# Kernel tuning notes

Hardware: AMD Instinct MI355X
Metric: run time of the kernel (lower is better)

Reference implementation:

```python
import jax, jax.numpy as jnp
import numpy as np

B, LC, LQ, D = 64, 1024, 128, 128
NEG_BIG = 1.0e12


def _len_mask(seq_len, T):
    # seq_len: (B,1) int. Equivalent to 1 - cumsum(one_hot(L, T)): 1 for pos < L.
    pos = jnp.arange(T)  # (T,)
    return (pos[None, :] < seq_len).astype(jnp.float32)  # (B,T)


def setup_inputs() -> dict:
    key = jax.random.key(0)
    ks = jax.random.split(key, 7)
    return {
        "x_cont": jax.random.normal(ks[0], (B, LC, D), dtype=jnp.float32),
        "x_ques": jax.random.normal(ks[1], (B, LQ, D), dtype=jnp.float32),
        "W0": jax.random.normal(ks[2], (D, 1), dtype=jnp.float32) / np.sqrt(D),
        "W1": jax.random.normal(ks[3], (D, 1), dtype=jnp.float32) / np.sqrt(D),
        "W2": jax.random.normal(ks[4], (1, 1, D), dtype=jnp.float32) / np.sqrt(D),
        "cont_len": jax.random.randint(ks[5], (B, 1), 1, LC, dtype=jnp.int32),
        "ques_len": jax.random.randint(ks[6], (B, 1), 1, LQ, dtype=jnp.int32),
    }


def reference(x_cont, x_ques, W0, W1, W2, cont_len, ques_len):
    # Trilinear similarity: S[b,c,q] = x_cont@W0 + x_ques@W1 + (x_cont*W2) . x_ques
    s_cont = jnp.einsum('bcd,do->bco', x_cont, W0)            # (B,LC,1)
    s_ques = jnp.einsum('bqd,do->boq', x_ques, W1)            # (B,1,LQ)
    s_fuse = jnp.einsum('bcd,bqd->bcq', x_cont * W2, x_ques)  # (B,LC,LQ)
    S = s_cont + s_ques + s_fuse                               # (B,LC,LQ)

    mask_q = _len_mask(ques_len, LQ)  # (B,LQ)
    mask_c = _len_mask(cont_len, LC)  # (B,LC)

    # Softmax over query axis, masking invalid query positions (axis=-1)
    S_bar = jax.nn.softmax(S - (1.0 - mask_q)[:, None, :] * NEG_BIG, axis=-1)
    # Softmax over context axis, masking invalid context positions, then transpose
    S_T = jnp.swapaxes(
        jax.nn.softmax(S - (1.0 - mask_c)[:, :, None] * NEG_BIG, axis=1), 1, 2
    )  # (B,LQ,LC)

    c2q = jnp.einsum('bcq,bqd->bcd', S_bar, x_ques)             # (B,LC,D)
    q2c = jnp.einsum('bcq,bqk,bkd->bcd', S_bar, S_T, x_cont)    # (B,LC,D)

    result = jnp.concatenate(
        [x_cont, c2q, x_cont * c2q, x_cont * q2c], axis=-1
    )  # (B,LC,4D)
    return result, S_bar, S_T
```

## Files before the change

kernel.cpp:

```cpp
#include <hip/hip_runtime.h>

#define NB 64
#define LC 1024
#define LQ 128
#define DD 128
#define NEG_BIG 1.0e12f

typedef __attribute__((ext_vector_type(8))) short short8;
typedef __attribute__((ext_vector_type(4))) unsigned short ushort4v;
typedef __attribute__((ext_vector_type(4))) float floatx4;

__device__ __forceinline__ unsigned short f2bf(float f) {
  union { float f; unsigned int u; } v;
  v.f = f;
  const unsigned int r = v.u + 0x7FFFu + ((v.u >> 16) & 1u);
  return (unsigned short)(r >> 16);
}
__device__ __forceinline__ float bf2f(unsigned int u) {
  union { unsigned int u; float f; } v;
  v.u = u << 16;
  return v.f;
}

#define PADW 136

__global__ __launch_bounds__(512) void k_score(
    const float* __restrict__ xc, const float* __restrict__ xq,
    const float* __restrict__ w2, const float* __restrict__ W0,
    const float* __restrict__ W1, const int* __restrict__ qlen_p,
    const int* __restrict__ clen_p, float* __restrict__ out_sbar,
    unsigned short* __restrict__ Pb, float* __restrict__ colsum_part,
    unsigned short* __restrict__ xcT, unsigned short* __restrict__ xqT,
    unsigned short* __restrict__ sbarb) {
  __shared__ __align__(16) unsigned short smem[2 * 128 * PADW];
  __shared__ float a_cont_s[128];
  __shared__ float a_ques_s[128];
  unsigned short* xcs = smem;
  unsigned short* xqs = smem + 128 * PADW;
  unsigned short* ptile = smem + 128 * PADW;

  const int b = blockIdx.x >> 3;
  const int ct = blockIdx.x & 7;
  const int c0 = ct << 7;
  const int t = threadIdx.x;
  const int w = t >> 6, lane = t & 63;
  const int frow = lane & 15;
  const int kb = lane >> 4;

  const float* xc_blk = xc + ((size_t)b * LC + c0) * DD;
  const float* xq_b = xq + (size_t)b * LQ * DD;

  const int u = t & 15;
  const float4 w0a = *(const float4*)(W0 + (u << 3));
  const float4 w0b = *(const float4*)(W0 + (u << 3) + 4);
  const float4 w1a = *(const float4*)(W1 + (u << 3));
  const float4 w1b = *(const float4*)(W1 + (u << 3) + 4);
  const float4 w2a = *(const float4*)(w2 + (u << 3));
  const float4 w2b = *(const float4*)(w2 + (u << 3) + 4);

#pragma unroll
  for (int i = 0; i < 4; ++i) {
    const int row = (t >> 4) + (i << 5);
    {
      const float4 v0 = *(const float4*)(xc_blk + (size_t)row * DD + (u << 3));
      const float4 v1 = *(const float4*)(xc_blk + (size_t)row * DD + (u << 3) + 4);
      short8 pk;
      pk[0] = (short)f2bf(v0.x); pk[1] = (short)f2bf(v0.y);
      pk[2] = (short)f2bf(v0.z); pk[3] = (short)f2bf(v0.w);
      pk[4] = (short)f2bf(v1.x); pk[5] = (short)f2bf(v1.y);
      pk[6] = (short)f2bf(v1.z); pk[7] = (short)f2bf(v1.w);
      *(short8*)(xcs + row * PADW + (u << 3)) = pk;
      float pd = v0.x * w0a.x + v0.y * w0a.y + v0.z * w0a.z + v0.w * w0a.w +
                 v1.x * w0b.x + v1.y * w0b.y + v1.z * w0b.z + v1.w * w0b.w;
#pragma unroll
      for (int msk = 8; msk >= 1; msk >>= 1) pd += __shfl_xor(pd, msk, 64);
      if ((lane & 15) == 0) a_cont_s[row] = pd;
    }
    {
      const float4 v0 = *(const float4*)(xq_b + (size_t)row * DD + (u << 3));
      const float4 v1 = *(const float4*)(xq_b + (size_t)row * DD + (u << 3) + 4);
      float pq = v0.x * w1a.x + v0.y * w1a.y + v0.z * w1a.z + v0.w * w1a.w +
                 v1.x * w1b.x + v1.y * w1b.y + v1.z * w1b.z + v1.w * w1b.w;
#pragma unroll
      for (int msk = 8; msk >= 1; msk >>= 1) pq += __shfl_xor(pq, msk, 64);
      if ((lane & 15) == 0) a_ques_s[row] = pq;
      short8 pk;
      pk[0] = (short)f2bf(v0.x * w2a.x); pk[1] = (short)f2bf(v0.y * w2a.y);
      pk[2] = (short)f2bf(v0.z * w2a.z); pk[3] = (short)f2bf(v0.w * w2a.w);
      pk[4] = (short)f2bf(v1.x * w2b.x); pk[5] = (short)f2bf(v1.y * w2b.y);
      pk[6] = (short)f2bf(v1.z * w2b.z); pk[7] = (short)f2bf(v1.w * w2b.w);
      *(short8*)(xqs + row * PADW + (u << 3)) = pk;
    }
  }

  const int qlen = qlen_p[b];
  const int clen = clen_p[b];

  __syncthreads();

  float ac[4], aq[8];
#pragma unroll
  for (int reg = 0; reg < 4; ++reg)
    ac[reg] = a_cont_s[w * 16 + kb * 4 + reg];
#pragma unroll
  for (int n = 0; n < 8; ++n) aq[n] = a_ques_s[n * 16 + frow];

  floatx4 acc[8];
#pragma unroll
  for (int n = 0; n < 8; ++n) acc[n] = (floatx4){0.f, 0.f, 0.f, 0.f};
  const unsigned short* arow = xcs + (w * 16 + frow) * PADW + kb * 8;
  const unsigned short* brow = xqs + frow * PADW + kb * 8;
#pragma unroll
  for (int ks = 0; ks < 4; ++ks) {
    const short8 af = *(const short8*)(arow + ks * 32);
#pragma unroll
    for (int n = 0; n < 8; ++n) {
      const short8 bf = *(const short8*)(brow + n * 16 * PADW + ks * 32);
      acc[n] = __builtin_amdgcn_mfma_f32_16x16x32_bf16(af, bf, acc[n], 0, 0, 0);
    }
  }

  {
    const int d = t & 127;
    const int half = t >> 7;
    __align__(16) unsigned short tmp[32];
#pragma unroll
    for (int j = 0; j < 32; ++j)
      tmp[j] = xcs[((half << 5) + j) * PADW + d];
    unsigned short* dp = xcT + ((size_t)b * DD + d) * LC + c0 + (half << 5);
#pragma unroll
    for (int j = 0; j < 4; ++j)
      *(short8*)(dp + (j << 3)) = *(const short8*)(tmp + (j << 3));
  }

  float raw[8][4];
#pragma unroll
  for (int n = 0; n < 8; ++n)
#pragma unroll
    for (int reg = 0; reg < 4; ++reg) raw[n][reg] = acc[n][reg] + ac[reg] + aq[n];

  float mreg[4], invreg[4];
  float* sbar_row0 =
      out_sbar + ((size_t)b * LC + c0 + w * 16 + kb * 4) * LQ + frow;
#pragma unroll
  for (int reg = 0; reg < 4; ++reg) {
    float x[8];
    float m = -3.4e38f;
#pragma unroll
    for (int n = 0; n < 8; ++n) {
      x[n] = raw[n][reg] - ((n * 16 + frow) < qlen ? 0.f : NEG_BIG);
      m = fmaxf(m, x[n]);
    }
#pragma unroll
    for (int msk = 8; msk >= 1; msk >>= 1) m = fmaxf(m, __shfl_xor(m, msk, 64));
    float s = 0.f;
#pragma unroll
    for (int n = 0; n < 8; ++n) {
      x[n] = __expf(x[n] - m);
      s += x[n];
    }
#pragma unroll
    for (int msk = 8; msk >= 1; msk >>= 1) s += __shfl_xor(s, msk, 64);
    const float inv = 1.0f / s;
    float* o = sbar_row0 + (size_t)reg * LQ;
#pragma unroll
    for (int n = 0; n < 8; ++n) o[n * 16] = x[n] * inv;
    mreg[reg] = m;
    invreg[reg] = inv;
  }

  unsigned short* sb_out = sbarb + ((size_t)b * LC + c0) * LQ;
#pragma unroll
  for (int p = 0; p < 4; ++p) {
    __syncthreads();
    if ((w >> 1) == p) {
      const int crow = ((w & 1) << 4) + (kb << 2);
#pragma unroll
      for (int reg = 0; reg < 4; ++reg) {
        const float m = mreg[reg], inv = invreg[reg];
#pragma unroll
        for (int n = 0; n < 8; ++n) {
          const float xv = raw[n][reg] - ((n * 16 + frow) < qlen ? 0.f : NEG_BIG);
          ptile[(crow + reg) * 136 + (n << 4) + frow] = f2bf(__expf(xv - m) * inv);
        }
      }
    }
    __syncthreads();
    const int row = t >> 4, ch = t & 15;
    *(short8*)(sb_out + (size_t)((p << 5) + row) * LQ + (ch << 3)) =
        *(const short8*)(ptile + row * 136 + (ch << 3));
  }

  const int cl0 = c0 + w * 16 + kb * 4;
#pragma unroll
  for (int reg = 0; reg < 4; ++reg) {
    const bool ok = (cl0 + reg) < clen;
#pragma unroll
    for (int n = 0; n < 8; ++n)
      raw[n][reg] = ok ? __expf(raw[n][reg]) : 0.f;
  }

  unsigned short* Pb_b = Pb + (size_t)b * LQ * LC;
  float* cs_blk = colsum_part + ((size_t)b * 8 + ct) * LQ;
#pragma unroll
  for (int p = 0; p < 4; ++p) {
    __syncthreads();
#pragma unroll
    for (int n2 = 0; n2 < 2; ++n2) {
#pragma unroll
      for (int reg = 0; reg < 4; ++reg)
        ptile[(n2 * 16 + frow) * 136 + (w * 16 + kb * 4 + reg)] =
            f2bf(raw[2 * p + n2][reg]);
    }
    __syncthreads();
    const int qrow = t >> 4;
    const int ch = t & 15;
    const short8 pv = *(const short8*)(ptile + qrow * 136 + (ch << 3));
    *(short8*)(Pb_b + (size_t)(p * 32 + qrow) * LC + c0 + (ch << 3)) = pv;
    float s = 0.f;
#pragma unroll
    for (int j = 0; j < 8; ++j) s += bf2f((unsigned short)pv[j]);
#pragma unroll
    for (int msk = 8; msk >= 1; msk >>= 1) s += __shfl_xor(s, msk, 64);
    if (ch == 0) cs_blk[p * 32 + qrow] = s;
  }

  if (ct == 0) {
    __syncthreads();
#pragma unroll
    for (int i = 0; i < 4; ++i) {
      const int id = t + (i << 9);
      const int row = id >> 4, uu = id & 15;
      const float4 v0 = *(const float4*)(xq_b + (size_t)row * DD + (uu << 3));
      const float4 v1 = *(const float4*)(xq_b + (size_t)row * DD + (uu << 3) + 4);
      short8 pk;
      pk[0] = (short)f2bf(v0.x); pk[1] = (short)f2bf(v0.y);
      pk[2] = (short)f2bf(v0.z); pk[3] = (short)f2bf(v0.w);
      pk[4] = (short)f2bf(v1.x); pk[5] = (short)f2bf(v1.y);
      pk[6] = (short)f2bf(v1.z); pk[7] = (short)f2bf(v1.w);
      *(short8*)(ptile + row * 136 + (uu << 3)) = pk;
    }
    __syncthreads();
    const int d = t >> 2, ch4 = t & 3;
    __align__(16) unsigned short tmp2[32];
#pragma unroll
    for (int j = 0; j < 32; ++j)
      tmp2[j] = ptile[(ch4 * 32 + j) * 136 + d];
    unsigned short* dp = xqT + ((size_t)b * DD + d) * LQ + ch4 * 32;
#pragma unroll
    for (int j = 0; j < 4; ++j)
      *(short8*)(dp + (j << 3)) = *(const short8*)(tmp2 + (j << 3));
  }
}

__global__ __launch_bounds__(256) void k_fuse(
    const unsigned short* __restrict__ Pb, const float* __restrict__ colsum_part,
    const unsigned short* __restrict__ xcT, float* __restrict__ st,
    unsigned short* __restrict__ AbT) {
  __shared__ __align__(16) unsigned short Ps[16 * 1032];
  __shared__ unsigned short abt[128 * 20];
  __shared__ float inv_s[16];

  const int b = blockIdx.x >> 3;
  const int q0 = (blockIdx.x & 7) << 4;
  const int t = threadIdx.x;
  const int w = t >> 6, lane = t & 63;
  const int frow = lane & 15, kb = lane >> 4;

  const unsigned short* Pb_blk = Pb + ((size_t)b * LQ + q0) * LC;
  {
    const int row = t >> 4;
#pragma unroll
    for (int j = 0; j < 8; ++j) {
      const int cs = ((t & 15) << 3) + (j << 7);
      *(short8*)(Ps + row * 1032 + cs) =
          *(const short8*)(Pb_blk + (size_t)row * LC + cs);
    }
  }
  if (t < 16) {
    float s = 0.f;
#pragma unroll
    for (int j = 0; j < 8; ++j)
      s += colsum_part[((size_t)b * 8 + j) * LQ + q0 + t];
    inv_s[t] = 1.0f / s;
  }
  __syncthreads();

  {
    const int row = t >> 4;
    const float inv = inv_s[row];
    float* dst = st + ((size_t)b * LQ + q0 + row) * LC;
#pragma unroll
    for (int j = 0; j < 8; ++j) {
      const int cs = ((t & 15) << 3) + (j << 7);
      const short8 pv = *(const short8*)(Ps + row * 1032 + cs);
      float4 o0, o1;
      o0.x = bf2f((unsigned short)pv[0]) * inv;
      o0.y = bf2f((unsigned short)pv[1]) * inv;
      o0.z = bf2f((unsigned short)pv[2]) * inv;
      o0.w = bf2f((unsigned short)pv[3]) * inv;
      o1.x = bf2f((unsigned short)pv[4]) * inv;
      o1.y = bf2f((unsigned short)pv[5]) * inv;
      o1.z = bf2f((unsigned short)pv[6]) * inv;
      o1.w = bf2f((unsigned short)pv[7]) * inv;
      *(float4*)(dst + cs) = o0;
      *(float4*)(dst + cs + 4) = o1;
    }
  }

  const unsigned short* xcT_b = xcT + (size_t)b * DD * LC;
  const unsigned short* b0p =
      xcT_b + (size_t)((w * 2 + 0) * 16 + frow) * LC + kb * 8;
  const unsigned short* b1p =
      xcT_b + (size_t)((w * 2 + 1) * 16 + frow) * LC + kb * 8;
  const unsigned short* ap = Ps + frow * 1032 + kb * 8;
  floatx4 acc0 = (floatx4){0.f, 0.f, 0.f, 0.f};
  floatx4 acc1 = (floatx4){0.f, 0.f, 0.f, 0.f};
#pragma unroll 8
  for (int kk = 0; kk < 32; ++kk) {
    const short8 af = *(const short8*)(ap + kk * 32);
    const short8 b0 = *(const short8*)(b0p + kk * 32);
    const short8 b1 = *(const short8*)(b1p + kk * 32);
    acc0 = __builtin_amdgcn_mfma_f32_16x16x32_bf16(af, b0, acc0, 0, 0, 0);
    acc1 = __builtin_amdgcn_mfma_f32_16x16x32_bf16(af, b1, acc1, 0, 0, 0);
  }

  __syncthreads();
  const float i0 = inv_s[kb * 4 + 0], i1 = inv_s[kb * 4 + 1];
  const float i2 = inv_s[kb * 4 + 2], i3 = inv_s[kb * 4 + 3];
  {
    const int d0 = (w * 2 + 0) * 16 + frow;
    abt[d0 * 20 + kb * 4 + 0] = f2bf(acc0[0] * i0);
    abt[d0 * 20 + kb * 4 + 1] = f2bf(acc0[1] * i1);
    abt[d0 * 20 + kb * 4 + 2] = f2bf(acc0[2] * i2);
    abt[d0 * 20 + kb * 4 + 3] = f2bf(acc0[3] * i3);
    const int d1 = (w * 2 + 1) * 16 + frow;
    abt[d1 * 20 + kb * 4 + 0] = f2bf(acc1[0] * i0);
    abt[d1 * 20 + kb * 4 + 1] = f2bf(acc1[1] * i1);
    abt[d1 * 20 + kb * 4 + 2] = f2bf(acc1[2] * i2);
    abt[d1 * 20 + kb * 4 + 3] = f2bf(acc1[3] * i3);
  }
  __syncthreads();
  const int d = t >> 1, h = t & 1;
  short8 ov;
#pragma unroll
  for (int j = 0; j < 8; ++j)
    ((unsigned short*)&ov)[j] = abt[d * 20 + h * 8 + j];
  *(short8*)(AbT + ((size_t)b * DD + d) * LQ + q0 + h * 8) = ov;
}

__global__ __launch_bounds__(256) void k_out(
    const float* __restrict__ xc, const unsigned short* __restrict__ sbarb,
    const unsigned short* __restrict__ xqT, const unsigned short* __restrict__ AbT,
    float* __restrict__ out) {
  __shared__ __align__(16) float stg[2 * 32 * 132];

  const int b = blockIdx.x >> 4;
  const int c0 = (blockIdx.x & 15) << 6;
  const int t = threadIdx.x;
  const int w = t >> 6, lane = t & 63;
  const int frow = lane & 15, kb = lane >> 4;

  const unsigned short* sb_blk = sbarb + ((size_t)b * LC + c0) * LQ;
  const unsigned short* xqT_b = xqT + (size_t)b * DD * LQ;
  const unsigned short* AbT_b = AbT + (size_t)b * DD * LQ;
  short8 bq[2][4], ba[2][4];
#pragma unroll
  for (int nt = 0; nt < 2; ++nt) {
    const int d = (w << 5) + (nt << 4) + frow;
#pragma unroll
    for (int ks = 0; ks < 4; ++ks) {
      bq[nt][ks] = *(const short8*)(xqT_b + (size_t)d * LQ + ks * 32 + kb * 8);
      ba[nt][ks] = *(const short8*)(AbT_b + (size_t)d * LQ + ks * 32 + kb * 8);
    }
  }

  floatx4 accq[4][2], acca[4][2];
#pragma unroll
  for (int mt = 0; mt < 4; ++mt)
#pragma unroll
    for (int nt = 0; nt < 2; ++nt) {
      accq[mt][nt] = (floatx4){0.f, 0.f, 0.f, 0.f};
      acca[mt][nt] = (floatx4){0.f, 0.f, 0.f, 0.f};
    }
#pragma unroll
  for (int mt = 0; mt < 4; ++mt) {
#pragma unroll
    for (int ks = 0; ks < 4; ++ks) {
      const short8 af = *(const short8*)(
          sb_blk + (size_t)((mt << 4) + frow) * LQ + ks * 32 + kb * 8);
#pragma unroll
      for (int nt = 0; nt < 2; ++nt) {
        accq[mt][nt] =
            __builtin_amdgcn_mfma_f32_16x16x32_bf16(af, bq[nt][ks], accq[mt][nt], 0, 0, 0);
        acca[mt][nt] =
            __builtin_amdgcn_mfma_f32_16x16x32_bf16(af, ba[nt][ks], acca[mt][nt], 0, 0, 0);
      }
    }
  }

  float* out_b = out + ((size_t)b * LC + c0) * (4 * DD);
  const float* xc_blk = xc + ((size_t)b * LC + c0) * DD;

#pragma unroll
  for (int p = 0; p < 2; ++p) {
    __syncthreads();
#pragma unroll
    for (int mh = 0; mh < 2; ++mh) {
      const int mt = 2 * p + mh;
#pragma unroll
      for (int nt = 0; nt < 2; ++nt) {
        const int d = (w << 5) + (nt << 4) + frow;
        const int cl = (mh << 4) + (kb << 2);
#pragma unroll
        for (int reg = 0; reg < 4; ++reg) {
          stg[(cl + reg) * 132 + d] = accq[mt][nt][reg];
          stg[32 * 132 + (cl + reg) * 132 + d] = acca[mt][nt][reg];
        }
      }
    }
    __syncthreads();
    const int g = lane >> 4;
    const int d0 = (lane & 15) << 3;
#pragma unroll
    for (int j = 0; j < 8; ++j) {
      const int rl = (w << 3) + j;
      const int c = (p << 5) + rl;
      const float4 xv0 = *(const float4*)(xc_blk + (size_t)c * DD + d0);
      const float4 xv1 = *(const float4*)(xc_blk + (size_t)c * DD + d0 + 4);
      const float4 cq0 = *(const float4*)(stg + rl * 132 + d0);
      const float4 cq1 = *(const float4*)(stg + rl * 132 + d0 + 4);
      const float4 qc0 = *(const float4*)(stg + 32 * 132 + rl * 132 + d0);
      const float4 qc1 = *(const float4*)(stg + 32 * 132 + rl * 132 + d0 + 4);
      float4 o0, o1;
      if (g == 0) { o0 = xv0; o1 = xv1; }
      else if (g == 1) { o0 = cq0; o1 = cq1; }
      else if (g == 2) {
        o0 = make_float4(xv0.x * cq0.x, xv0.y * cq0.y, xv0.z * cq0.z, xv0.w * cq0.w);
        o1 = make_float4(xv1.x * cq1.x, xv1.y * cq1.y, xv1.z * cq1.z, xv1.w * cq1.w);
      } else {
        o0 = make_float4(xv0.x * qc0.x, xv0.y * qc0.y, xv0.z * qc0.z, xv0.w * qc0.w);
        o1 = make_float4(xv1.x * qc1.x, xv1.y * qc1.y, xv1.z * qc1.z, xv1.w * qc1.w);
      }
      float* o = out_b + (size_t)c * (4 * DD) + (g << 7) + d0;
      *(float4*)(o) = o0;
      *(float4*)(o + 4) = o1;
    }
  }
}

extern "C" void kernel_launch(void* const* d_in, const int* in_sizes, int n_in,
                              void* d_out, int out_size, void* d_ws, size_t ws_size,
                              hipStream_t stream) {
  const float* xc = (const float*)d_in[0];
  const float* xq = (const float*)d_in[1];
  const float* W0 = (const float*)d_in[2];
  const float* W1 = (const float*)d_in[3];
  const float* W2 = (const float*)d_in[4];
  const int* clen = (const int*)d_in[5];
  const int* qlen = (const int*)d_in[6];

  float* out = (float*)d_out;
  float* out_sbar = out + (size_t)NB * LC * 4 * DD;
  float* out_st = out_sbar + (size_t)NB * LC * LQ;

  float* colsum_part = (float*)d_ws;
  unsigned short* xcT = (unsigned short*)(colsum_part + NB * 8 * LQ);
  unsigned short* xqT = xcT + (size_t)NB * LC * DD;
  unsigned short* AbT = xqT + (size_t)NB * LQ * DD;
  unsigned short* Pb = AbT + (size_t)NB * LQ * DD;
  unsigned short* sbarb = Pb + (size_t)NB * LQ * LC;

  k_score<<<NB * 8, 512, 0, stream>>>(xc, xq, W2, W0, W1, qlen, clen,
                                      out_sbar, Pb, colsum_part, xcT, xqT,
                                      sbarb);
  k_fuse<<<NB * 8, 256, 0, stream>>>(Pb, colsum_part, xcT, out_st, AbT);
  k_out<<<NB * 16, 256, 0, stream>>>(xc, sbarb, xqT, AbT, out);
}
```

Before: 114.6 us.

## Coalesce S_bar and P stores via single LDS tile, move xqT transpose to k_fuse

The S_bar softmax epilogue now stages the whole 128x128 bf16 tile in LDS once and writes both the bf16 copy and the fp32 output with row-contiguous vector stores. Previously the fp32 store was strided per lane and the bf16 store went through four staged passes. The P/column-sum writeback likewise uses one full-tile LDS transpose with fewer barriers. The x_ques transpose that only ct==0 blocks did is moved into k_fuse, split across all blocks, to remove the load imbalance in k_score. The fp32 S_bar output is now derived from bf16-rounded values, which loses precision.

Result: slower. 127.4 us (+11.2%).

```diff
diff --git a/kernel.cpp b/kernel.cpp
--- a/kernel.cpp
+++ b/kernel.cpp
@@ -30,8 +30,7 @@
     const float* __restrict__ W1, const int* __restrict__ qlen_p,
     const int* __restrict__ clen_p, float* __restrict__ out_sbar,
     unsigned short* __restrict__ Pb, float* __restrict__ colsum_part,
-    unsigned short* __restrict__ xcT, unsigned short* __restrict__ xqT,
-    unsigned short* __restrict__ sbarb) {
+    unsigned short* __restrict__ xcT, unsigned short* __restrict__ sbarb) {
   __shared__ __align__(16) unsigned short smem[2 * 128 * PADW];
   __shared__ float a_cont_s[128];
   __shared__ float a_ques_s[128];
@@ -140,8 +139,6 @@
     for (int reg = 0; reg < 4; ++reg) raw[n][reg] = acc[n][reg] + ac[reg] + aq[n];
 
   float mreg[4], invreg[4];
-  float* sbar_row0 =
-      out_sbar + ((size_t)b * LC + c0 + w * 16 + kb * 4) * LQ + frow;
 #pragma unroll
   for (int reg = 0; reg < 4; ++reg) {
     float x[8];
@@ -155,40 +152,42 @@
     for (int msk = 8; msk >= 1; msk >>= 1) m = fmaxf(m, __shfl_xor(m, msk, 64));
     float s = 0.f;
 #pragma unroll
+    for (int n = 0; n < 8; ++n) s += __expf(x[n] - m);
+#pragma unroll
+    for (int msk = 8; msk >= 1; msk >>= 1) s += __shfl_xor(s, msk, 64);
+    mreg[reg] = m;
+    invreg[reg] = 1.0f / s;
+  }
+
+  __syncthreads();
+#pragma unroll
+  for (int reg = 0; reg < 4; ++reg) {
+    const int crow = w * 16 + kb * 4 + reg;
+    const float m = mreg[reg], inv = invreg[reg];
+#pragma unroll
     for (int n = 0; n < 8; ++n) {
-      x[n] = __expf(x[n] - m);
-      s += x[n];
-    }
-#pragma unroll
-    for (int msk = 8; msk >= 1; msk >>= 1) s += __shfl_xor(s, msk, 64);
-    const float inv = 1.0f / s;
-    float* o = sbar_row0 + (size_t)reg * LQ;
-#pragma unroll
-    for (int n = 0; n < 8; ++n) o[n * 16] = x[n] * inv;
-    mreg[reg] = m;
-    invreg[reg] = inv;
-  }
-
-  unsigned short* sb_out = sbarb + ((size_t)b * LC + c0) * LQ;
-#pragma unroll
-  for (int p = 0; p < 4; ++p) {
-    __syncthreads();
-    if ((w >> 1) == p) {
-      const int crow = ((w & 1) << 4) + (kb << 2);
-#pragma unroll
-      for (int reg = 0; reg < 4; ++reg) {
-        const float m = mreg[reg], inv = invreg[reg];
-#pragma unroll
-        for (int n = 0; n < 8; ++n) {
-          const float xv = raw[n][reg] - ((n * 16 + frow) < qlen ? 0.f : NEG_BIG);
-          ptile[(crow + reg) * 136 + (n << 4) + frow] = f2bf(__expf(xv - m) * inv);
-        }
-      }
-    }
-    __syncthreads();
-    const int row = t >> 4, ch = t & 15;
-    *(short8*)(sb_out + (size_t)((p << 5) + row) * LQ + (ch << 3)) =
-        *(const short8*)(ptile + row * 136 + (ch << 3));
+      const float xv = raw[n][reg] - ((n * 16 + frow) < qlen ? 0.f : NEG_BIG);
+      ptile[crow * 136 + (n << 4) + frow] = f2bf(__expf(xv - m) * inv);
+    }
+  }
+  __syncthreads();
+  {
+    const int row = t >> 2;
+    const int ch = t & 3;
+    unsigned short* sb_out = sbarb + ((size_t)b * LC + c0 + row) * LQ + (ch << 5);
+    float* sf_out = out_sbar + ((size_t)b * LC + c0 + row) * LQ + (ch << 5);
+#pragma unroll
+    for (int k = 0; k < 4; ++k) {
+      const short8 v = *(const short8*)(ptile + row * 136 + (ch << 5) + (k << 3));
+      *(short8*)(sb_out + (k << 3)) = v;
+      float4 f0, f1;
+      f0.x = bf2f((unsigned short)v[0]); f0.y = bf2f((unsigned short)v[1]);
+      f0.z = bf2f((unsigned short)v[2]); f0.w = bf2f((unsigned short)v[3]);
+      f1.x = bf2f((unsigned short)v[4]); f1.y = bf2f((unsigned short)v[5]);
+      f1.z = bf2f((unsigned short)v[6]); f1.w = bf2f((unsigned short)v[7]);
+      *(float4*)(sf_out + (k << 3)) = f0;
+      *(float4*)(sf_out + (k << 3) + 4) = f1;
+    }
   }
 
   const int cl0 = c0 + w * 16 + kb * 4;
@@ -200,66 +199,42 @@
       raw[n][reg] = ok ? __expf(raw[n][reg]) : 0.f;
   }
 
-  unsigned short* Pb_b = Pb + (size_t)b * LQ * LC;
-  float* cs_blk = colsum_part + ((size_t)b * 8 + ct) * LQ;
-#pragma unroll
-  for (int p = 0; p < 4; ++p) {
-    __syncthreads();
-#pragma unroll
-    for (int n2 = 0; n2 < 2; ++n2) {
-#pragma unroll
-      for (int reg = 0; reg < 4; ++reg)
-        ptile[(n2 * 16 + frow) * 136 + (w * 16 + kb * 4 + reg)] =
-            f2bf(raw[2 * p + n2][reg]);
-    }
-    __syncthreads();
-    const int qrow = t >> 4;
-    const int ch = t & 15;
-    const short8 pv = *(const short8*)(ptile + qrow * 136 + (ch << 3));
-    *(short8*)(Pb_b + (size_t)(p * 32 + qrow) * LC + c0 + (ch << 3)) = pv;
+  __syncthreads();
+#pragma unroll
+  for (int n = 0; n < 8; ++n) {
+#pragma unroll
+    for (int reg = 0; reg < 4; ++reg)
+      ptile[((n << 4) + frow) * 136 + w * 16 + kb * 4 + reg] =
+          f2bf(raw[n][reg]);
+  }
+  __syncthreads();
+  {
+    const int row = t >> 2;
+    const int ch = t & 3;
+    unsigned short* dst = Pb + ((size_t)b * LQ + row) * LC + c0 + (ch << 5);
     float s = 0.f;
 #pragma unroll
-    for (int j = 0; j < 8; ++j) s += bf2f((unsigned short)pv[j]);
-#pragma unroll
-    for (int msk = 8; msk >= 1; msk >>= 1) s += __shfl_xor(s, msk, 64);
-    if (ch == 0) cs_blk[p * 32 + qrow] = s;
-  }
-
-  if (ct == 0) {
-    __syncthreads();
-#pragma unroll
-    for (int i = 0; i < 4; ++i) {
-      const int id = t + (i << 9);
-      const int row = id >> 4, uu = id & 15;
-      const float4 v0 = *(const float4*)(xq_b + (size_t)row * DD + (uu << 3));
-      const float4 v1 = *(const float4*)(xq_b + (size_t)row * DD + (uu << 3) + 4);
-      short8 pk;
-      pk[0] = (short)f2bf(v0.x); pk[1] = (short)f2bf(v0.y);
-      pk[2] = (short)f2bf(v0.z); pk[3] = (short)f2bf(v0.w);
-      pk[4] = (short)f2bf(v1.x); pk[5] = (short)f2bf(v1.y);
-      pk[6] = (short)f2bf(v1.z); pk[7] = (short)f2bf(v1.w);
-      *(short8*)(ptile + row * 136 + (uu << 3)) = pk;
-    }
-    __syncthreads();
-    const int d = t >> 2, ch4 = t & 3;
-    __align__(16) unsigned short tmp2[32];
-#pragma unroll
-    for (int j = 0; j < 32; ++j)
-      tmp2[j] = ptile[(ch4 * 32 + j) * 136 + d];
-    unsigned short* dp = xqT + ((size_t)b * DD + d) * LQ + ch4 * 32;
-#pragma unroll
-    for (int j = 0; j < 4; ++j)
-      *(short8*)(dp + (j << 3)) = *(const short8*)(tmp2 + (j << 3));
+    for (int k = 0; k < 4; ++k) {
+      const short8 v = *(const short8*)(ptile + row * 136 + (ch << 5) + (k << 3));
+      *(short8*)(dst + (k << 3)) = v;
+#pragma unroll
+      for (int j = 0; j < 8; ++j) s += bf2f((unsigned short)v[j]);
+    }
+    s += __shfl_xor(s, 1, 64);
+    s += __shfl_xor(s, 2, 64);
+    if (ch == 0) colsum_part[((size_t)b * 8 + ct) * LQ + row] = s;
   }
 }
 
 __global__ __launch_bounds__(256) void k_fuse(
     const unsigned short* __restrict__ Pb, const float* __restrict__ colsum_part,
-    const unsigned short* __restrict__ xcT, float* __restrict__ st,
+    const unsigned short* __restrict__ xcT, const float* __restrict__ xq,
+    float* __restrict__ st, unsigned short* __restrict__ xqT,
     unsigned short* __restrict__ AbT) {
   __shared__ __align__(16) unsigned short Ps[16 * 1032];
-  __shared__ unsigned short abt[128 * 20];
+  __shared__ __align__(16) unsigned short abt[128 * 20];
   __shared__ float inv_s[16];
+  unsigned short* xqtile = abt;
 
   const int b = blockIdx.x >> 3;
   const int q0 = (blockIdx.x & 7) << 4;
@@ -277,6 +252,19 @@
           *(const short8*)(Pb_blk + (size_t)row * LC + cs);
     }
   }
+  {
+    const int qrow = t >> 4, dch = t & 15;
+    const float4 v0 =
+        *(const float4*)(xq + ((size_t)b * LQ + q0 + qrow) * DD + (dch << 3));
+    const float4 v1 =
+        *(const float4*)(xq + ((size_t)b * LQ + q0 + qrow) * DD + (dch << 3) + 4);
+    short8 pk;
+    pk[0] = (short)f2bf(v0.x); pk[1] = (short)f2bf(v0.y);
+    pk[2] = (short)f2bf(v0.z); pk[3] = (short)f2bf(v0.w);
+    pk[4] = (short)f2bf(v1.x); pk[5] = (short)f2bf(v1.y);
+    pk[6] = (short)f2bf(v1.z); pk[7] = (short)f2bf(v1.w);
+    *(short8*)(xqtile + qrow * 136 + (dch << 3)) = pk;
+  }
   if (t < 16) {
     float s = 0.f;
 #pragma unroll
@@ -285,6 +273,16 @@
     inv_s[t] = 1.0f / s;
   }
   __syncthreads();
+
+  {
+    const int d = t >> 1, half = t & 1;
+    __align__(16) unsigned short tmp[8];
+#pragma unroll
+    for (int j = 0; j < 8; ++j)
+      tmp[j] = xqtile[((half << 3) + j) * 136 + d];
+    *(short8*)(xqT + ((size_t)b * DD + d) * LQ + q0 + (half << 3)) =
+        *(const short8*)(tmp);
+  }
 
   {
     const int row = t >> 4;
@@ -472,8 +470,8 @@
   unsigned short* sbarb = Pb + (size_t)NB * LQ * LC;
 
   k_score<<<NB * 8, 512, 0, stream>>>(xc, xq, W2, W0, W1, qlen, clen,
-                                      out_sbar, Pb, colsum_part, xcT, xqT,
-                                      sbarb);
-  k_fuse<<<NB * 8, 256, 0, stream>>>(Pb, colsum_part, xcT, out_st, AbT);
+                                      out_sbar, Pb, colsum_part, xcT, sbarb);
+  k_fuse<<<NB * 8, 256, 0, stream>>>(Pb, colsum_part, xcT, xq, out_st, xqT,
+                                     AbT);
   k_out<<<NB * 16, 256, 0, stream>>>(xc, sbarb, xqT, AbT, out);
 }
```
